# Kernel optimization log

Hardware: AMD Instinct MI355X
Metric: run time of the kernel (lower is better)

The kernel has to match this reference:

```python
import jax, jax.numpy as jnp
import numpy as np

DIM, HEADS, SEG, DIL = 1024, 16, 64, 2
B, L = 4, 4096
HEAD_DIM = DIM // HEADS
SCALE = HEAD_DIM ** -0.5


def _hilbert_map(seq_len: int) -> np.ndarray:
    # exact port of generate_hilbert_curve / hilbert_index
    size = int(np.ceil(np.sqrt(seq_len)))
    if size * size != seq_len:
        size = 2 ** int(np.ceil(np.log2(size)))

    def hidx(x, y, n):
        d = 0
        s = n // 2
        while s > 0:
            rx = 1 if (x & s) > 0 else 0
            ry = 1 if (y & s) > 0 else 0
            d += s * s * ((3 * rx) ^ ry)
            if ry == 0:
                if rx == 1:
                    x = n - 1 - x
                    y = n - 1 - y
                x, y = y, x
            s //= 2
        return d

    m = np.zeros(size * size, dtype=np.int32)
    for y in range(size):
        for x in range(size):
            m[y * size + x] = hidx(x, y, size)
    return m[:seq_len]


def setup_inputs() -> dict:
    key = jax.random.key(0)
    k1, k2, k3 = jax.random.split(key, 3)
    x = jax.random.normal(k1, (B, L, DIM), dtype=jnp.float32)
    w_qkv = jax.random.normal(k2, (DIM, 3 * DIM), dtype=jnp.float32) * 0.02
    w_proj = jax.random.normal(k3, (DIM, DIM), dtype=jnp.float32) * 0.02
    hilbert_map = jnp.asarray(_hilbert_map(L))
    return {"x": x, "w_qkv": w_qkv, "w_proj": w_proj, "hilbert_map": hilbert_map}


def reference(x, w_qkv, w_proj, hilbert_map):
    Bq, Lq, _ = x.shape
    n_seg = Lq // SEG
    # qkv projection -> [3, B, H, L, D]
    qkv = (x @ w_qkv).reshape(Bq, Lq, 3, HEADS, HEAD_DIM).transpose(2, 0, 3, 1, 4)
    q, k, v = qkv[0], qkv[1], qkv[2]
    # Hilbert reorder along sequence
    q = q[:, :, hilbert_map, :]
    k = k[:, :, hilbert_map, :]
    v = v[:, :, hilbert_map, :]
    # segmented dilated attention: [B,H,S,seg,D]
    qs = q.reshape(Bq, HEADS, n_seg, SEG, HEAD_DIM)
    ks = k.reshape(Bq, HEADS, n_seg, SEG, HEAD_DIM)[:, :, :, ::DIL, :]
    vs = v.reshape(Bq, HEADS, n_seg, SEG, HEAD_DIM)[:, :, :, ::DIL, :]
    scores = jnp.einsum('bhsqd,bhskd->bhsqk', qs, ks) * SCALE
    attn = jax.nn.softmax(scores, axis=-1)
    out = jnp.einsum('bhsqk,bhskd->bhsqd', attn, vs).reshape(Bq, HEADS, Lq, HEAD_DIM)
    # inverse Hilbert reorder
    inv = jnp.argsort(hilbert_map)
    out = out[:, :, inv, :]
    out = out.transpose(0, 2, 1, 3).reshape(Bq, Lq, DIM)
    return out @ w_proj
```

## Files before the change

### kernel.cpp

```cpp
#include <hip/hip_runtime.h>

#define L_SEQ 4096

typedef unsigned short u16;
typedef unsigned int u32;
typedef __bf16 bf16_t;
typedef bf16_t bf16x8 __attribute__((ext_vector_type(8)));
typedef float f32x4 __attribute__((ext_vector_type(4)));
typedef unsigned short u16x8 __attribute__((ext_vector_type(8)));

__device__ __forceinline__ u16 f2b(float f) {
  unsigned u = __float_as_uint(f);
  u += 0x7fffu + ((u >> 16) & 1u);
  return (u16)(u >> 16);
}
__device__ __forceinline__ float b2f(u16 b) {
  return __uint_as_float(((unsigned)b) << 16);
}

#define FENCE asm volatile("" ::: "memory")
#define BARRIER __builtin_amdgcn_s_barrier()
#define WAIT_LGKM0 asm volatile("s_waitcnt lgkmcnt(0)" ::: "memory")
#define WAIT_VM4 asm volatile("s_waitcnt vmcnt(4)" ::: "memory")
#define SB0 __builtin_amdgcn_sched_barrier(0)
#define AS1 __attribute__((address_space(1)))
#define AS3 __attribute__((address_space(3)))

__global__ __launch_bounds__(256) void k_prep(const float* __restrict__ x,
                                              u16* __restrict__ xb,
                                              const float* __restrict__ wq,
                                              u16* __restrict__ wqT,
                                              const float* __restrict__ wp,
                                              u16* __restrict__ wpT) {
  const int bid = blockIdx.x;
  const int t = threadIdx.x;
  if (bid < 4096) {
    const int i = (bid * 256 + t) * 16;
    f32x4 v0 = *reinterpret_cast<const f32x4*>(x + i);
    f32x4 v1 = *reinterpret_cast<const f32x4*>(x + i + 4);
    f32x4 v2 = *reinterpret_cast<const f32x4*>(x + i + 8);
    f32x4 v3 = *reinterpret_cast<const f32x4*>(x + i + 12);
    u16x8 o0, o1;
#pragma unroll
    for (int j = 0; j < 4; ++j) {
      o0[j] = f2b(v0[j]); o0[4 + j] = f2b(v1[j]);
      o1[j] = f2b(v2[j]); o1[4 + j] = f2b(v3[j]);
    }
    *reinterpret_cast<u16x8*>(xb + i) = o0;
    *reinterpret_cast<u16x8*>(xb + i + 8) = o1;
    return;
  }
  const float* in; u16* out; int R, C, bx, by;
  if (bid < 7168) {
    const int b2 = bid - 4096;
    in = wq; out = wqT; R = 1024; C = 3072;
    bx = (b2 % 96) * 32; by = (b2 / 96) * 32;
  } else {
    const int b2 = bid - 7168;
    in = wp; out = wpT; R = 1024; C = 1024;
    bx = (b2 % 32) * 32; by = (b2 / 32) * 32;
  }
  __shared__ float tile[32][33];
  const int tx = t & 31, ty = t >> 5;
#pragma unroll
  for (int i = 0; i < 32; i += 8)
    tile[ty + i][tx] = in[(size_t)(by + ty + i) * C + (bx + tx)];
  __syncthreads();
#pragma unroll
  for (int i = 0; i < 32; i += 8)
    out[(size_t)(bx + ty + i) * R + (by + tx)] = f2b(tile[tx][ty + i]);
}

template <bool OUT_BF16, bool AMAP>
__device__ __forceinline__ void gemm_body(char* lds, const u16* __restrict__ A,
                                          const u16* __restrict__ Bt,
                                          const int* __restrict__ hmap,
                                          void* __restrict__ Cv,
                                          int N, int K, int gx, int bid) {
  const int tid = threadIdx.x;
  const int wid = tid >> 6, lane = tid & 63;
  const int wm = wid >> 2, wn = wid & 3;
  const int lr = lane & 15, lq = lane >> 4;
  const int xr = (lr & 7) << 4;
  const int koff0 = (lq * 16) ^ xr;
  const int koff1 = (64 | (lq * 16)) ^ xr;

  const int swz = (bid & 7) * 32 + (bid >> 3);
  const int m0 = (swz / gx) * 256, n0 = (swz % gx) * 256;

  const int rowT = tid >> 3;
  const int colT = (((tid * 16) & 127) ^ ((rowT & 7) << 4)) >> 1;
  const size_t r64K = (size_t)64 * K;
  const size_t r128K = (size_t)128 * K;

  const u16 *pA0, *pA1, *pA2, *pA3;
  if constexpr (AMAP) {
    auto maprow = [&](int gi) -> const u16* {
      const int token = hmap[((gi & 2047) >> 5) * 64 + 2 * (gi & 31)];
      return A + ((size_t)((gi >> 11) * 4096 + token)) * (size_t)K + colT;
    };
    pA0 = maprow(m0 + rowT);
    pA1 = maprow(m0 + 64 + rowT);
    pA2 = maprow(m0 + 128 + rowT);
    pA3 = maprow(m0 + 192 + rowT);
  } else {
    pA0 = A + (size_t)(m0 + rowT) * K + colT;
    pA1 = pA0 + r64K; pA2 = pA0 + r128K; pA3 = pA2 + r64K;
  }
  const u16* pBc = Bt + (size_t)(n0 + rowT) * K + colT;

  f32x4 acc[8][4];
  bf16x8 a[4][2];
  bf16x8 bb[2][2][2];

  auto LDS1 = [&](const u16* s0, int region) {
    __builtin_amdgcn_global_load_lds((const AS1 void*)s0,
                                     (AS3 void*)(lds + region + wid * 1024), 16, 0, 0);
  };
  auto STG_A0 = [&](int region, int k0) {
    LDS1(pA0 + k0, region); LDS1(pA1 + k0, region + 8192);
  };
  auto STG_A1 = [&](int region, int k0) {
    LDS1(pA2 + k0, region); LDS1(pA3 + k0, region + 8192);
  };
  auto STG_B = [&](int region, size_t hoff, int k0) {
    LDS1(pBc + hoff + k0, region); LDS1(pBc + hoff + r64K + k0, region + 8192);
  };
  auto rdA = [&](int dbuf, int mh) {
#pragma unroll
    for (int mi = 0; mi < 4; ++mi) {
      const int base = dbuf * 65536 + wm * 16384 + (mh * 64 + mi * 16 + lr) * 128;
      a[mi][0] = *(const bf16x8*)(lds + base + koff0);
      a[mi][1] = *(const bf16x8*)(lds + base + koff1);
    }
  };
  auto rdB = [&](int dbuf, int nh, int bset) {
#pragma unroll
    for (int ni = 0; ni < 2; ++ni) {
      const int base = dbuf * 65536 + 32768 + (wn >> 1) * 16384 +
                       ((wn & 1) * 64 + nh * 32 + ni * 16 + lr) * 128;
      bb[bset][ni][0] = *(const bf16x8*)(lds + base + koff0);
      bb[bset][ni][1] = *(const bf16x8*)(lds + base + koff1);
    }
  };
  auto mfma16 = [&](int mh, int nh, int bset) {
    __builtin_amdgcn_s_setprio(1);
#pragma unroll
    for (int kk = 0; kk < 2; ++kk)
#pragma unroll
      for (int ni = 0; ni < 2; ++ni)
#pragma unroll
        for (int mi = 0; mi < 4; ++mi)
          acc[mh * 4 + mi][nh * 2 + ni] = __builtin_amdgcn_mfma_f32_16x16x32_bf16(
              a[mi][kk], bb[bset][ni][kk], acc[mh * 4 + mi][nh * 2 + ni], 0, 0, 0);
    __builtin_amdgcn_s_setprio(0);
  };

  {
    f32x4 z = {0.f, 0.f, 0.f, 0.f};
#pragma unroll
    for (int i = 0; i < 8; ++i)
#pragma unroll
      for (int j = 0; j < 4; ++j) acc[i][j] = z;
  }

  STG_A0(0, 0);
  STG_B(32768, 0, 0);
  STG_B(49152, r128K, 0);
  STG_A1(16384, 0);
  STG_B(65536 + 32768, 0, 64);
  STG_B(65536 + 49152, r128K, 64);
  WAIT_VM4; FENCE; BARRIER;

  const int NI = K >> 7;

  for (int it = 0; it < NI; ++it) {
    const int kP1 = (2 * it + 1) * 64;
    const bool last = (it == NI - 1);
    const int kA = last ? 0 : (2 * it + 2) * 64;
    const int kB = last ? 64 : (2 * it + 3) * 64;

    rdA(0, 0); rdB(0, 0, 0);
    STG_A0(65536, kP1);
    FENCE; BARRIER; WAIT_LGKM0; SB0;
    mfma16(0, 0, 0);
    FENCE; BARRIER;
    rdB(0, 1, 1);
    STG_A1(65536 + 16384, kP1);
    FENCE; BARRIER; WAIT_LGKM0; SB0;
    mfma16(0, 1, 1);
    FENCE; BARRIER;
    rdA(0, 1);
    STG_B(32768, 0, kA);
    STG_B(49152, r128K, kA);
    FENCE; BARRIER; WAIT_LGKM0; SB0;
    mfma16(1, 1, 1);
    mfma16(1, 0, 0);
    WAIT_VM4; FENCE; BARRIER;
    rdA(1, 0); rdB(1, 0, 0);
    STG_A0(0, kA);
    FENCE; BARRIER; WAIT_LGKM0; SB0;
    mfma16(0, 0, 0);
    FENCE; BARRIER;
    rdB(1, 1, 1);
    STG_A1(16384, kA);
    FENCE; BARRIER; WAIT_LGKM0; SB0;
    mfma16(0, 1, 1);
    FENCE; BARRIER;
    rdA(1, 1);
    STG_B(65536 + 32768, 0, kB);
    STG_B(65536 + 49152, r128K, kB);
    FENCE; BARRIER; WAIT_LGKM0; SB0;
    mfma16(1, 1, 1);
    mfma16(1, 0, 0);
    WAIT_VM4; FENCE; BARRIER;
  }

#pragma unroll
  for (int mi = 0; mi < 8; ++mi)
#pragma unroll
    for (int ni = 0; ni < 4; ++ni) {
      const int r0 = m0 + wm * 128 + (mi >> 2) * 64 + (mi & 3) * 16 + lq * 4;
      const int c = n0 + wn * 64 + (ni >> 1) * 32 + (ni & 1) * 16 + lr;
#pragma unroll
      for (int r = 0; r < 4; ++r) {
        const float v = acc[mi][ni][r];
        if (OUT_BF16)
          ((u16*)Cv)[(size_t)(r0 + r) * N + c] = f2b(v);
        else
          ((float*)Cv)[(size_t)(r0 + r) * N + c] = v;
      }
    }
}

__global__ __launch_bounds__(512, 2) void k_gemm_qkv(const u16* __restrict__ xb,
                                                     const u16* __restrict__ wT,
                                                     const int* __restrict__ hmap,
                                                     u16* __restrict__ qb,
                                                     u16* __restrict__ kvb) {
  __shared__ __align__(16) char lds[131072];
  if (blockIdx.x >= 256)
    gemm_body<true, true>(lds, xb, wT + 1024 * 1024, hmap, kvb, 2048, 1024, 8,
                          blockIdx.x & 255);
  else
    gemm_body<true, false>(lds, xb, wT, nullptr, qb, 1024, 1024, 4, blockIdx.x);
}

__global__ __launch_bounds__(512, 2) void k_gemm_proj(const u16* __restrict__ A,
                                                      const u16* __restrict__ Bt,
                                                      float* __restrict__ C) {
  __shared__ __align__(16) char lds[131072];
  gemm_body<false, false>(lds, A, Bt, nullptr, C, 1024, 1024, 4, blockIdx.x);
}

__global__ __launch_bounds__(256) void k_attn2(const u16* __restrict__ qb,
                                               const u16* __restrict__ kvb,
                                               const int* __restrict__ hmap,
                                               u16* __restrict__ att) {
  __shared__ u16 VT[64 * 40];
  __shared__ u16 Pl[4][16 * 40];

  const int blk = blockIdx.x;
  const int b = blk >> 10, h = (blk >> 6) & 15, s = blk & 63;
  const int t = threadIdx.x, w = t >> 6, lane = t & 63;
  const int lr = lane & 15, lq = lane >> 4;
  const int* hm = hmap + s * 64;
  const size_t bb4 = (size_t)b * L_SEQ;
  const size_t kvrow0 = (size_t)(b * 2048 + s * 32);

  {
    const int kj = t >> 3, d0 = (t & 7) * 8;
    const u16* p = kvb + (kvrow0 + kj) * 2048 + 1024 + h * 64 + d0;
    u16x8 v = *(const u16x8*)p;
#pragma unroll
    for (int j = 0; j < 8; ++j) {
      const int d = d0 + j;
      const int chunk = (kj >> 3) ^ ((d >> 3) & 3);
      VT[d * 40 + chunk * 8 + (kj & 7)] = v[j];
    }
  }

  const u16* qp = qb + (bb4 + hm[16 * w + lr]) * 1024 + h * 64 + lq * 8;
  bf16x8 aq0 = *(const bf16x8*)(qp);
  bf16x8 aq1 = *(const bf16x8*)(qp + 32);
  bf16x8 bk[2][2];
#pragma unroll
  for (int nk = 0; nk < 2; ++nk) {
    const u16* kp = kvb + (kvrow0 + nk * 16 + lr) * 2048 + h * 64 + lq * 8;
    bk[nk][0] = *(const bf16x8*)(kp);
    bk[nk][1] = *(const bf16x8*)(kp + 32);
  }

  f32x4 z4 = {0.f, 0.f, 0.f, 0.f};
  f32x4 s0 = __builtin_amdgcn_mfma_f32_16x16x32_bf16(aq0, bk[0][0], z4, 0, 0, 0);
  s0 = __builtin_amdgcn_mfma_f32_16x16x32_bf16(aq1, bk[0][1], s0, 0, 0, 0);
  f32x4 s1 = __builtin_amdgcn_mfma_f32_16x16x32_bf16(aq0, bk[1][0], z4, 0, 0, 0);
  s1 = __builtin_amdgcn_mfma_f32_16x16x32_bf16(aq1, bk[1][1], s1, 0, 0, 0);

  float inv[4];
  u16* Pw = Pl[w];
#pragma unroll
  for (int r = 0; r < 4; ++r) {
    float a0 = s0[r] * 0.125f, a1 = s1[r] * 0.125f;
    float m = fmaxf(a0, a1);
    m = fmaxf(m, __shfl_xor(m, 1));
    m = fmaxf(m, __shfl_xor(m, 2));
    m = fmaxf(m, __shfl_xor(m, 4));
    m = fmaxf(m, __shfl_xor(m, 8));
    float e0 = __expf(a0 - m), e1 = __expf(a1 - m);
    float sum = e0 + e1;
    sum += __shfl_xor(sum, 1);
    sum += __shfl_xor(sum, 2);
    sum += __shfl_xor(sum, 4);
    sum += __shfl_xor(sum, 8);
    inv[r] = 1.f / sum;
    Pw[(lq * 4 + r) * 40 + lr] = f2b(e0);
    Pw[(lq * 4 + r) * 40 + 16 + lr] = f2b(e1);
  }

  __syncthreads();

  bf16x8 ap = *(const bf16x8*)(Pw + lr * 40 + lq * 8);
  f32x4 o[4];
#pragma unroll
  for (int nd = 0; nd < 4; ++nd) {
    const int row = nd * 16 + lr;
    const int chunk = lq ^ ((row >> 3) & 3);
    bf16x8 bv = *(const bf16x8*)(VT + row * 40 + chunk * 8);
    o[nd] = __builtin_amdgcn_mfma_f32_16x16x32_bf16(ap, bv, z4, 0, 0, 0);
  }

#pragma unroll
  for (int r = 0; r < 4; ++r) {
    u16* dst = att + (bb4 + hm[16 * w + lq * 4 + r]) * 1024 + h * 64 + lr;
#pragma unroll
    for (int nd = 0; nd < 4; ++nd)
      dst[nd * 16] = f2b(o[nd][r] * inv[r]);
  }
}

extern "C" void kernel_launch(void* const* d_in, const int* in_sizes, int n_in,
                              void* d_out, int out_size, void* d_ws, size_t ws_size,
                              hipStream_t stream) {
  const float* x = (const float*)d_in[0];
  const float* w_qkv = (const float*)d_in[1];
  const float* w_proj = (const float*)d_in[2];
  const int* hmap = (const int*)d_in[3];
  float* out = (float*)d_out;

  char* ws = (char*)d_ws;
  u16* qb    = (u16*)(ws);
  u16* kvb   = (u16*)(ws + 33554432ull);
  u16* xb    = (u16*)(ws + 67108864ull);
  u16* wqkvT = (u16*)(ws + 100663296ull);
  u16* wpT   = (u16*)(ws + 106954752ull);
  u16* att = xb;

  k_prep<<<8192, 256, 0, stream>>>(x, xb, w_qkv, wqkvT, w_proj, wpT);
  k_gemm_qkv<<<512, 512, 0, stream>>>(xb, wqkvT, hmap, qb, kvb);
  k_attn2<<<4096, 256, 0, stream>>>(qb, kvb, hmap, att);
  k_gemm_proj<<<256, 512, 0, stream>>>(att, wpT, out);
}
```

Baseline: 154.6 us.

## Make QKV GEMM persistent: each block computes Q and KV tiles with cross-tile prefetch

```diff
diff --git a/kernel.cpp b/kernel.cpp
--- a/kernel.cpp
+++ b/kernel.cpp
@@ -71,12 +71,14 @@
     out[(size_t)(bx + ty + i) * R + (by + tx)] = f2b(tile[tx][ty + i]);
 }
 
-template <bool OUT_BF16, bool AMAP>
-__device__ __forceinline__ void gemm_body(char* lds, const u16* __restrict__ A,
-                                          const u16* __restrict__ Bt,
-                                          const int* __restrict__ hmap,
-                                          void* __restrict__ Cv,
-                                          int N, int K, int gx, int bid) {
+struct TD {
+  const u16 *a0, *a1, *a2, *a3;
+  const u16 *b;
+  char* dst; int N, m0, n0;
+};
+
+template <bool OUT_BF16, int NT>
+__device__ __forceinline__ void gemm_body(char* lds, const TD* td, int K) {
   const int tid = threadIdx.x;
   const int wid = tid >> 6, lane = tid & 63;
   const int wm = wid >> 2, wn = wid & 3;
@@ -84,47 +86,28 @@
   const int xr = (lr & 7) << 4;
   const int koff0 = (lq * 16) ^ xr;
   const int koff1 = (64 | (lq * 16)) ^ xr;
-
-  const int swz = (bid & 7) * 32 + (bid >> 3);
-  const int m0 = (swz / gx) * 256, n0 = (swz % gx) * 256;
-
-  const int rowT = tid >> 3;
-  const int colT = (((tid * 16) & 127) ^ ((rowT & 7) << 4)) >> 1;
   const size_t r64K = (size_t)64 * K;
   const size_t r128K = (size_t)128 * K;
 
-  const u16 *pA0, *pA1, *pA2, *pA3;
-  if constexpr (AMAP) {
-    auto maprow = [&](int gi) -> const u16* {
-      const int token = hmap[((gi & 2047) >> 5) * 64 + 2 * (gi & 31)];
-      return A + ((size_t)((gi >> 11) * 4096 + token)) * (size_t)K + colT;
-    };
-    pA0 = maprow(m0 + rowT);
-    pA1 = maprow(m0 + 64 + rowT);
-    pA2 = maprow(m0 + 128 + rowT);
-    pA3 = maprow(m0 + 192 + rowT);
-  } else {
-    pA0 = A + (size_t)(m0 + rowT) * K + colT;
-    pA1 = pA0 + r64K; pA2 = pA0 + r128K; pA3 = pA2 + r64K;
-  }
-  const u16* pBc = Bt + (size_t)(n0 + rowT) * K + colT;
-
   f32x4 acc[8][4];
   bf16x8 a[4][2];
-  bf16x8 bb[2][2][2];
+  bf16x8 bbf[2][2][2];
 
   auto LDS1 = [&](const u16* s0, int region) {
     __builtin_amdgcn_global_load_lds((const AS1 void*)s0,
                                      (AS3 void*)(lds + region + wid * 1024), 16, 0, 0);
   };
-  auto STG_A0 = [&](int region, int k0) {
-    LDS1(pA0 + k0, region); LDS1(pA1 + k0, region + 8192);
-  };
-  auto STG_A1 = [&](int region, int k0) {
-    LDS1(pA2 + k0, region); LDS1(pA3 + k0, region + 8192);
-  };
-  auto STG_B = [&](int region, size_t hoff, int k0) {
-    LDS1(pBc + hoff + k0, region); LDS1(pBc + hoff + r64K + k0, region + 8192);
+  auto stgA0 = [&](const u16* p0, const u16* p1, int k0, int dbuf) {
+    LDS1(p0 + k0, dbuf * 65536); LDS1(p1 + k0, dbuf * 65536 + 8192);
+  };
+  auto stgA1 = [&](const u16* p2, const u16* p3, int k0, int dbuf) {
+    LDS1(p2 + k0, dbuf * 65536 + 16384); LDS1(p3 + k0, dbuf * 65536 + 24576);
+  };
+  auto stgB = [&](const u16* bp, int k0, int dbuf) {
+    LDS1(bp + k0, dbuf * 65536 + 32768);
+    LDS1(bp + r64K + k0, dbuf * 65536 + 40960);
+    LDS1(bp + r128K + k0, dbuf * 65536 + 49152);
+    LDS1(bp + r128K + r64K + k0, dbuf * 65536 + 57344);
   };
   auto rdA = [&](int dbuf, int mh) {
 #pragma unroll
@@ -139,8 +122,8 @@
     for (int ni = 0; ni < 2; ++ni) {
       const int base = dbuf * 65536 + 32768 + (wn >> 1) * 16384 +
                        ((wn & 1) * 64 + nh * 32 + ni * 16 + lr) * 128;
-      bb[bset][ni][0] = *(const bf16x8*)(lds + base + koff0);
-      bb[bset][ni][1] = *(const bf16x8*)(lds + base + koff1);
+      bbf[bset][ni][0] = *(const bf16x8*)(lds + base + koff0);
+      bbf[bset][ni][1] = *(const bf16x8*)(lds + base + koff1);
     }
   };
   auto mfma16 = [&](int mh, int nh, int bset) {
@@ -152,85 +135,92 @@
 #pragma unroll
         for (int mi = 0; mi < 4; ++mi)
           acc[mh * 4 + mi][nh * 2 + ni] = __builtin_amdgcn_mfma_f32_16x16x32_bf16(
-              a[mi][kk], bb[bset][ni][kk], acc[mh * 4 + mi][nh * 2 + ni], 0, 0, 0);
+              a[mi][kk], bbf[bset][ni][kk], acc[mh * 4 + mi][nh * 2 + ni], 0, 0, 0);
     __builtin_amdgcn_s_setprio(0);
   };
 
-  {
-    f32x4 z = {0.f, 0.f, 0.f, 0.f};
-#pragma unroll
-    for (int i = 0; i < 8; ++i)
-#pragma unroll
-      for (int j = 0; j < 4; ++j) acc[i][j] = z;
-  }
-
-  STG_A0(0, 0);
-  STG_B(32768, 0, 0);
-  STG_B(49152, r128K, 0);
-  STG_A1(16384, 0);
-  STG_B(65536 + 32768, 0, 64);
-  STG_B(65536 + 49152, r128K, 64);
+  stgA0(td[0].a0, td[0].a1, 0, 0);
+  stgB(td[0].b, 0, 0);
+  stgA1(td[0].a2, td[0].a3, 0, 0);
+  stgB(td[0].b, 64, 1);
   WAIT_VM4; FENCE; BARRIER;
 
   const int NI = K >> 7;
 
-  for (int it = 0; it < NI; ++it) {
-    const int kP1 = (2 * it + 1) * 64;
-    const bool last = (it == NI - 1);
-    const int kA = last ? 0 : (2 * it + 2) * 64;
-    const int kB = last ? 64 : (2 * it + 3) * 64;
-
-    rdA(0, 0); rdB(0, 0, 0);
-    STG_A0(65536, kP1);
-    FENCE; BARRIER; WAIT_LGKM0; SB0;
-    mfma16(0, 0, 0);
-    FENCE; BARRIER;
-    rdB(0, 1, 1);
-    STG_A1(65536 + 16384, kP1);
-    FENCE; BARRIER; WAIT_LGKM0; SB0;
-    mfma16(0, 1, 1);
-    FENCE; BARRIER;
-    rdA(0, 1);
-    STG_B(32768, 0, kA);
-    STG_B(49152, r128K, kA);
-    FENCE; BARRIER; WAIT_LGKM0; SB0;
-    mfma16(1, 1, 1);
-    mfma16(1, 0, 0);
-    WAIT_VM4; FENCE; BARRIER;
-    rdA(1, 0); rdB(1, 0, 0);
-    STG_A0(0, kA);
-    FENCE; BARRIER; WAIT_LGKM0; SB0;
-    mfma16(0, 0, 0);
-    FENCE; BARRIER;
-    rdB(1, 1, 1);
-    STG_A1(16384, kA);
-    FENCE; BARRIER; WAIT_LGKM0; SB0;
-    mfma16(0, 1, 1);
-    FENCE; BARRIER;
-    rdA(1, 1);
-    STG_B(65536 + 32768, 0, kB);
-    STG_B(65536 + 49152, r128K, kB);
-    FENCE; BARRIER; WAIT_LGKM0; SB0;
-    mfma16(1, 1, 1);
-    mfma16(1, 0, 0);
-    WAIT_VM4; FENCE; BARRIER;
-  }
-
-#pragma unroll
-  for (int mi = 0; mi < 8; ++mi)
-#pragma unroll
-    for (int ni = 0; ni < 4; ++ni) {
-      const int r0 = m0 + wm * 128 + (mi >> 2) * 64 + (mi & 3) * 16 + lq * 4;
-      const int c = n0 + wn * 64 + (ni >> 1) * 32 + (ni & 1) * 16 + lr;
-#pragma unroll
-      for (int r = 0; r < 4; ++r) {
-        const float v = acc[mi][ni][r];
-        if (OUT_BF16)
-          ((u16*)Cv)[(size_t)(r0 + r) * N + c] = f2b(v);
-        else
-          ((float*)Cv)[(size_t)(r0 + r) * N + c] = v;
+#pragma unroll
+  for (int tt = 0; tt < NT; ++tt) {
+    const TD& cur = td[tt];
+    const TD& nxt = td[(tt + 1 < NT) ? (tt + 1) : (NT - 1)];
+
+    {
+      f32x4 z = {0.f, 0.f, 0.f, 0.f};
+#pragma unroll
+      for (int i = 0; i < 8; ++i)
+#pragma unroll
+        for (int j = 0; j < 4; ++j) acc[i][j] = z;
+    }
+
+    for (int it = 0; it < NI; ++it) {
+      const int kP1 = (2 * it + 1) * 64;
+      const bool last = (it == NI - 1);
+      const int kA = last ? 0 : (2 * it + 2) * 64;
+      const int kB = last ? 64 : (2 * it + 3) * 64;
+      const u16* sa0 = last ? nxt.a0 : cur.a0;
+      const u16* sa1 = last ? nxt.a1 : cur.a1;
+      const u16* sa2 = last ? nxt.a2 : cur.a2;
+      const u16* sa3 = last ? nxt.a3 : cur.a3;
+      const u16* sb  = last ? nxt.b  : cur.b;
+
+      rdA(0, 0); rdB(0, 0, 0);
+      stgA0(cur.a0, cur.a1, kP1, 1);
+      FENCE; BARRIER; WAIT_LGKM0; SB0;
+      mfma16(0, 0, 0);
+      FENCE; BARRIER;
+      rdB(0, 1, 1);
+      stgA1(cur.a2, cur.a3, kP1, 1);
+      FENCE; BARRIER; WAIT_LGKM0; SB0;
+      mfma16(0, 1, 1);
+      FENCE; BARRIER;
+      rdA(0, 1);
+      stgB(sb, kA, 0);
+      FENCE; BARRIER; WAIT_LGKM0; SB0;
+      mfma16(1, 1, 1);
+      mfma16(1, 0, 0);
+      WAIT_VM4; FENCE; BARRIER;
+      rdA(1, 0); rdB(1, 0, 0);
+      stgA0(sa0, sa1, kA, 0);
+      FENCE; BARRIER; WAIT_LGKM0; SB0;
+      mfma16(0, 0, 0);
+      FENCE; BARRIER;
+      rdB(1, 1, 1);
+      stgA1(sa2, sa3, kA, 0);
+      FENCE; BARRIER; WAIT_LGKM0; SB0;
+      mfma16(0, 1, 1);
+      FENCE; BARRIER;
+      rdA(1, 1);
+      stgB(sb, kB, 1);
+      FENCE; BARRIER; WAIT_LGKM0; SB0;
+      mfma16(1, 1, 1);
+      mfma16(1, 0, 0);
+      WAIT_VM4; FENCE; BARRIER;
+    }
+
+#pragma unroll
+    for (int mi = 0; mi < 8; ++mi)
+#pragma unroll
+      for (int ni = 0; ni < 4; ++ni) {
+        const int r0 = cur.m0 + wm * 128 + (mi >> 2) * 64 + (mi & 3) * 16 + lq * 4;
+        const int c = cur.n0 + wn * 64 + (ni >> 1) * 32 + (ni & 1) * 16 + lr;
+#pragma unroll
+        for (int r = 0; r < 4; ++r) {
+          const float v = acc[mi][ni][r];
+          if (OUT_BF16)
+            ((u16*)cur.dst)[(size_t)(r0 + r) * cur.N + c] = f2b(v);
+          else
+            ((float*)cur.dst)[(size_t)(r0 + r) * cur.N + c] = v;
+        }
       }
-    }
+  }
 }
 
 __global__ __launch_bounds__(512, 2) void k_gemm_qkv(const u16* __restrict__ xb,
@@ -239,18 +229,53 @@
                                                      u16* __restrict__ qb,
                                                      u16* __restrict__ kvb) {
   __shared__ __align__(16) char lds[131072];
-  if (blockIdx.x >= 256)
-    gemm_body<true, true>(lds, xb, wT + 1024 * 1024, hmap, kvb, 2048, 1024, 8,
-                          blockIdx.x & 255);
-  else
-    gemm_body<true, false>(lds, xb, wT, nullptr, qb, 1024, 1024, 4, blockIdx.x);
+  const int bid = blockIdx.x;
+  const int tid = threadIdx.x;
+  const int rowT = tid >> 3;
+  const int colT = (((tid * 16) & 127) ^ ((rowT & 7) << 4)) >> 1;
+  const int swz = (bid & 7) * 32 + (bid >> 3);
+
+  TD td[2];
+  {
+    const int m0 = (swz >> 2) * 256, n0 = (swz & 3) * 256;
+    const u16* ap = xb + (size_t)(m0 + rowT) * 1024 + colT;
+    td[0].a0 = ap; td[0].a1 = ap + 64 * 1024;
+    td[0].a2 = ap + 128 * 1024; td[0].a3 = ap + 192 * 1024;
+    td[0].b = wT + (size_t)(n0 + rowT) * 1024 + colT;
+    td[0].dst = (char*)qb; td[0].N = 1024; td[0].m0 = m0; td[0].n0 = n0;
+  }
+  {
+    const int m0 = (swz >> 3) * 256, n0 = (swz & 7) * 256;
+    auto maprow = [&](int gi) -> const u16* {
+      const int token = hmap[((gi & 2047) >> 5) * 64 + 2 * (gi & 31)];
+      return xb + ((size_t)((gi >> 11) * 4096 + token)) * 1024 + colT;
+    };
+    td[1].a0 = maprow(m0 + rowT); td[1].a1 = maprow(m0 + 64 + rowT);
+    td[1].a2 = maprow(m0 + 128 + rowT); td[1].a3 = maprow(m0 + 192 + rowT);
+    td[1].b = wT + 1024 * 1024 + (size_t)(n0 + rowT) * 1024 + colT;
+    td[1].dst = (char*)kvb; td[1].N = 2048; td[1].m0 = m0; td[1].n0 = n0;
+  }
+  gemm_body<true, 2>(lds, td, 1024);
 }
 
 __global__ __launch_bounds__(512, 2) void k_gemm_proj(const u16* __restrict__ A,
                                                       const u16* __restrict__ Bt,
                                                       float* __restrict__ C) {
   __shared__ __align__(16) char lds[131072];
-  gemm_body<false, false>(lds, A, Bt, nullptr, C, 1024, 1024, 4, blockIdx.x);
+  const int bid = blockIdx.x;
+  const int tid = threadIdx.x;
+  const int rowT = tid >> 3;
+  const int colT = (((tid * 16) & 127) ^ ((rowT & 7) << 4)) >> 1;
+  const int swz = (bid & 7) * 32 + (bid >> 3);
+  const int m0 = (swz >> 2) * 256, n0 = (swz & 3) * 256;
+  TD td[2];
+  const u16* ap = A + (size_t)(m0 + rowT) * 1024 + colT;
+  td[0].a0 = ap; td[0].a1 = ap + 64 * 1024;
+  td[0].a2 = ap + 128 * 1024; td[0].a3 = ap + 192 * 1024;
+  td[0].b = Bt + (size_t)(n0 + rowT) * 1024 + colT;
+  td[0].dst = (char*)C; td[0].N = 1024; td[0].m0 = m0; td[0].n0 = n0;
+  td[1] = td[0];
+  gemm_body<false, 1>(lds, td, 1024);
 }
 
 __global__ __launch_bounds__(256) void k_attn2(const u16* __restrict__ qb,
@@ -357,7 +382,7 @@
   u16* att = xb;
 
   k_prep<<<8192, 256, 0, stream>>>(x, xb, w_qkv, wqkvT, w_proj, wpT);
-  k_gemm_qkv<<<512, 512, 0, stream>>>(xb, wqkvT, hmap, qb, kvb);
+  k_gemm_qkv<<<256, 512, 0, stream>>>(xb, wqkvT, hmap, qb, kvb);
   k_attn2<<<4096, 256, 0, stream>>>(qb, kvb, hmap, att);
   k_gemm_proj<<<256, 512, 0, stream>>>(att, wpT, out);
 }
```

New measurement: 159.2 us. 3.0% more time.
